# Kernel tuning notes

Measured on AMD Instinct MI355X. Metric: run time of the kernel, lower is better.

The kernel has to match this reference:

```python
import jax, jax.numpy as jnp
import numpy as np

EPS = 1e-3
LOG2PI = float(np.log(2.0 * np.pi))

# dims
B, Z, Y, T, D = 32768, 256, 32, 64, 4  # batch, z_dim, y_dim, n_types, type_dim


def setup_inputs() -> dict:
    key = jax.random.key(0)
    ks = jax.random.split(key, 8)
    z = jax.random.normal(ks[0], (B, Z), dtype=jnp.float32)
    batch_x = jax.random.normal(ks[1], (B, T, D), dtype=jnp.float32)
    miss_list = jax.random.randint(ks[2], (B, T), 0, 2, dtype=jnp.int32)  # 1=observed, 0=missing
    data_mean = jax.random.normal(ks[3], (T, D), dtype=jnp.float32)
    data_var = jax.random.uniform(ks[4], (T, D), dtype=jnp.float32, minval=0.5, maxval=1.5)
    # weights init N(0, 0.005) as in the torch module; biases zero
    Wy = jax.random.normal(ks[5], (T * Y, Z), dtype=jnp.float32) * 0.005
    by = jnp.zeros((T * Y,), dtype=jnp.float32)
    Wm = jax.random.normal(ks[6], (T, D, Y), dtype=jnp.float32) * 0.005
    bm = jnp.zeros((T, D), dtype=jnp.float32)
    Wv = jax.random.normal(ks[7], (T, D, Y), dtype=jnp.float32) * 0.005
    bv = jnp.zeros((T, D), dtype=jnp.float32)
    return {"z": z, "batch_x": batch_x, "miss_list": miss_list,
            "data_mean": data_mean, "data_var": data_var,
            "Wy": Wy, "by": by, "Wm": Wm, "bm": bm, "Wv": Wv, "bv": bv}


def reference(z, batch_x, miss_list, data_mean, data_var, Wy, by, Wm, bm, Wv, bv):
    # y_layer: z -> [B, T*Y], grouped into per-type gamma slices [B, T, Y]
    y = z @ Wy.T + by
    gamma = y.reshape(y.shape[0], T, Y)

    mask = miss_list.astype(gamma.dtype)            # [B, T], 1=observed
    m3 = mask[:, :, None]                           # [B, T, 1]

    # per-type tiny linears (dynamic_partition + Linear + dynamic_stitch).
    # Numerically: same linear on all rows; missing rows are under no_grad,
    # realized here as stop_gradient on the missing partition.
    lin_m = jnp.einsum('bty,tdy->btd', gamma, Wm) + bm   # [B, T, D]
    lin_v = jnp.einsum('bty,tdy->btd', gamma, Wv) + bv
    est_mean = m3 * lin_m + (1.0 - m3) * jax.lax.stop_gradient(lin_m)
    est_var_raw = m3 * lin_v + (1.0 - m3) * jax.lax.stop_gradient(lin_v)

    # loglik_real: softplus variance, denormalize with data mean/var
    dvar = jnp.clip(data_var, EPS)
    est_var = jnp.clip(jax.nn.softplus(est_var_raw), EPS, 1e20)
    mean_x = jnp.sqrt(dvar) * est_mean + data_mean       # [B, T, D]
    var_x = dvar * est_var                               # [B, T, D]

    log_p = -0.5 * jnp.sum((batch_x - mean_x) ** 2 / var_x + jnp.log(var_x) + LOG2PI, axis=-1)  # [B, T]
    log_p_x = log_p * mask
    log_p_x_missing = log_p * (1.0 - mask)
    return (log_p_x, log_p_x_missing, mean_x, var_x)
```

## Files before the change

### kernel.cpp

```cpp
#include <hip/hip_runtime.h>


#define Bsz   32768
#define Tsz   64
#define Dsz   4
#define Ysz   32
#define Zsz   256
#define Nsz   512
#define BTtot (Bsz * Tsz)
#define EPS_  1e-3f
#define LOG2PI_ 1.8378770664093453f

#define BM       32
#define NT       512
#define ASTRIDE  264
#define LSTRIDE  524

typedef __attribute__((ext_vector_type(4))) float  f32x4;
typedef __attribute__((ext_vector_type(8))) short  short8;
typedef __attribute__((ext_vector_type(2))) unsigned int uint2v;

static __device__ __forceinline__ unsigned short f2bf(float f) {
    unsigned int u = __float_as_uint(f);
    return (unsigned short)((u + 0x7fffu + ((u >> 16) & 1u)) >> 16);
}
static __device__ __forceinline__ float bf2f(unsigned short h) {
    return __uint_as_float(((unsigned int)h) << 16);
}
static __device__ __forceinline__ unsigned int cvt_pk_bf16(float a, float b) {
    unsigned int r;
    asm("v_cvt_pk_bf16_f32 %0, %1, %2" : "=v"(r) : "v"(a), "v"(b));
    return r;
}

__global__ __launch_bounds__(256)
void hidec_prep(const float* __restrict__ Wy, const float* __restrict__ by,
                const float* __restrict__ Wm, const float* __restrict__ bm,
                const float* __restrict__ Wv, const float* __restrict__ bv,
                unsigned short* __restrict__ weff, float* __restrict__ beff) {
    __shared__ float Ml[8][Ysz];
    __shared__ float byl[Ysz];
    const int t   = blockIdx.x;
    const int tid = threadIdx.x;
    {
        int j = tid >> 5, y = tid & 31;
        const float* src = (j < 4) ? Wm : Wv;
        Ml[j][y] = src[(t * Dsz + (j & 3)) * Ysz + y];
    }
    if (tid < Ysz) byl[tid] = by[t * Ysz + tid];
    __syncthreads();

    const int k = tid;
    const int kk = k >> 5, q = (k >> 3) & 3, je = k & 7;
    float wy[Ysz];
#pragma unroll
    for (int y = 0; y < Ysz; ++y)
        wy[y] = Wy[(size_t)(t * Ysz + y) * Zsz + k];
#pragma unroll
    for (int j = 0; j < 8; ++j) {
        float acc = 0.f;
#pragma unroll
        for (int y = 0; y < Ysz; ++y) acc = fmaf(Ml[j][y], wy[y], acc);
        int n   = t * 8 + j;
        int tau = n >> 4, c = n & 15;
        weff[((((tau * 8 + kk) * 4 + q) * 16 + c) * 8) + je] = f2bf(acc);
    }
    if (tid < 8) {
        int d = tid & 3;
        float s = ((tid < 4) ? bm : bv)[t * Dsz + d];
        for (int y = 0; y < Ysz; ++y) s = fmaf(byl[y], Ml[tid][y], s);
        beff[t * 8 + tid] = s;
    }
}

__global__ __launch_bounds__(NT, 8)
void hidec_main(const float* __restrict__ z, const float* __restrict__ bx,
                const int* __restrict__ miss, const float* __restrict__ dmean,
                const float* __restrict__ dvarp, const unsigned short* __restrict__ weff,
                const float* __restrict__ beff, float* __restrict__ out) {
    __shared__ unsigned short buf[BM * LSTRIDE];

    const int tid  = threadIdx.x;
    const long row0 = (long)blockIdx.x * BM;

    unsigned short* a_lds = buf;
#pragma unroll
    for (int i = 0; i < 4; ++i) {
        int idx4 = tid + i * NT;
        int r  = idx4 >> 6;
        int c4 = idx4 & 63;
        float4 v = *(const float4*)(z + (row0 + r) * Zsz + c4 * 4);
        uint2v pk;
        pk.x = cvt_pk_bf16(v.x, v.y);
        pk.y = cvt_pk_bf16(v.z, v.w);
        *(uint2v*)&a_lds[r * ASTRIDE + c4 * 4] = pk;
    }
    __syncthreads();

    const int lane = tid & 63;
    const int w    = tid >> 6;
    const int c    = lane & 15;
    const int q    = lane >> 4;

    f32x4 acc[8];
#pragma unroll
    for (int i = 0; i < 8; ++i) acc[i] = (f32x4){0.f, 0.f, 0.f, 0.f};

    const unsigned short* wp = weff + ((size_t)(w * 4) * 8) * 512 + lane * 8;

#pragma unroll
    for (int kk = 0; kk < 8; ++kk) {
        short8 b0 = *(const short8*)(wp + kk * 512 + 0 * 4096);
        short8 b1 = *(const short8*)(wp + kk * 512 + 1 * 4096);
        short8 b2 = *(const short8*)(wp + kk * 512 + 2 * 4096);
        short8 b3 = *(const short8*)(wp + kk * 512 + 3 * 4096);
        short8 a0 = *(const short8*)&a_lds[(0 * 16 + c) * ASTRIDE + kk * 32 + q * 8];
        short8 a1 = *(const short8*)&a_lds[(1 * 16 + c) * ASTRIDE + kk * 32 + q * 8];
        acc[0] = __builtin_amdgcn_mfma_f32_16x16x32_bf16(a0, b0, acc[0], 0, 0, 0);
        acc[1] = __builtin_amdgcn_mfma_f32_16x16x32_bf16(a1, b0, acc[1], 0, 0, 0);
        acc[2] = __builtin_amdgcn_mfma_f32_16x16x32_bf16(a0, b1, acc[2], 0, 0, 0);
        acc[3] = __builtin_amdgcn_mfma_f32_16x16x32_bf16(a1, b1, acc[3], 0, 0, 0);
        acc[4] = __builtin_amdgcn_mfma_f32_16x16x32_bf16(a0, b2, acc[4], 0, 0, 0);
        acc[5] = __builtin_amdgcn_mfma_f32_16x16x32_bf16(a1, b2, acc[5], 0, 0, 0);
        acc[6] = __builtin_amdgcn_mfma_f32_16x16x32_bf16(a0, b3, acc[6], 0, 0, 0);
        acc[7] = __builtin_amdgcn_mfma_f32_16x16x32_bf16(a1, b3, acc[7], 0, 0, 0);
    }
    __syncthreads();

    unsigned short* lin = buf;
    {
        float bb[4];
#pragma unroll
        for (int ti = 0; ti < 4; ++ti) bb[ti] = beff[w * 64 + ti * 16 + c];
#pragma unroll
        for (int h = 0; h < 2; ++h) {
#pragma unroll
            for (int ti = 0; ti < 4; ++ti) {
                int cb = w * 64 + ti * 16 + c;
                const f32x4 a = acc[ti * 2 + h];
                unsigned int p01 = cvt_pk_bf16(a[0] + bb[ti], a[1] + bb[ti]);
                unsigned int p23 = cvt_pk_bf16(a[2] + bb[ti], a[3] + bb[ti]);
                int rbase = h * 16 + q * 4;
                lin[(rbase + 0) * LSTRIDE + cb] = (unsigned short)(p01 & 0xffffu);
                lin[(rbase + 1) * LSTRIDE + cb] = (unsigned short)(p01 >> 16);
                lin[(rbase + 2) * LSTRIDE + cb] = (unsigned short)(p23 & 0xffffu);
                lin[(rbase + 3) * LSTRIDE + cb] = (unsigned short)(p23 >> 16);
            }
        }
    }
    __syncthreads();

    const int t = lane;
    float4 dv4 = *(const float4*)(dvarp + t * 4);
    float4 dm4 = *(const float4*)(dmean + t * 4);
    float dca[4] = {fmaxf(dv4.x, EPS_), fmaxf(dv4.y, EPS_),
                    fmaxf(dv4.z, EPS_), fmaxf(dv4.w, EPS_)};
    float sqa[4] = {sqrtf(dca[0]), sqrtf(dca[1]), sqrtf(dca[2]), sqrtf(dca[3])};
    float dma[4] = {dm4.x, dm4.y, dm4.z, dm4.w};
    float sldv = __logf(dca[0]) + __logf(dca[1]) + __logf(dca[2]) + __logf(dca[3]);

#pragma unroll
    for (int pp = 0; pp < 4; ++pp) {
        int rl  = pp * 8 + w;
        long bt = (row0 + rl) * Tsz + t;

        short8 l8 = *(const short8*)&lin[rl * LSTRIDE + t * 8];
        float lm[4], lv[4];
#pragma unroll
        for (int d = 0; d < 4; ++d) {
            lm[d] = bf2f((unsigned short)l8[d]);
            lv[d] = bf2f((unsigned short)l8[4 + d]);
        }

        float4 x4  = *(const float4*)(bx + bt * 4);
        float mk   = (float)miss[bt];
        float xa[4]  = {x4.x,  x4.y,  x4.z,  x4.w};

        float mean_o[4], var_o[4];
        float s = sldv;
        float evp = 1.f;
#pragma unroll
        for (int d = 0; d < 4; ++d) {
            float mean = fmaf(sqa[d], lm[d], dma[d]);
            float v    = lv[d];
            float sp   = fmaxf(v, 0.f) + __logf(1.f + __expf(-fabsf(v)));
            float ev   = fminf(fmaxf(sp, EPS_), 1e20f);
            float var  = dca[d] * ev;
            float diff = xa[d] - mean;
            s = fmaf(diff * diff, __builtin_amdgcn_rcpf(var), s);
            evp *= ev;
            mean_o[d] = mean;
            var_o[d]  = var;
        }
        s += __logf(evp);
        float logp = -0.5f * (s + 4.f * LOG2PI_);

        float lx = logp * mk;
        out[bt]         = lx;
        out[BTtot + bt] = logp - lx;

        *(float4*)(out + 2L * BTtot + bt * 4) =
            (float4){mean_o[0], mean_o[1], mean_o[2], mean_o[3]};
        *(float4*)(out + 6L * BTtot + bt * 4) =
            (float4){var_o[0], var_o[1], var_o[2], var_o[3]};
    }
}

extern "C" void kernel_launch(void* const* d_in, const int* in_sizes, int n_in,
                              void* d_out, int out_size, void* d_ws, size_t ws_size,
                              hipStream_t stream) {
    const float* z     = (const float*)d_in[0];
    const float* bx    = (const float*)d_in[1];
    const int*   miss  = (const int*)d_in[2];
    const float* dmean = (const float*)d_in[3];
    const float* dvar  = (const float*)d_in[4];
    const float* Wy    = (const float*)d_in[5];
    const float* by    = (const float*)d_in[6];
    const float* Wm    = (const float*)d_in[7];
    const float* bm    = (const float*)d_in[8];
    const float* Wv    = (const float*)d_in[9];
    const float* bv    = (const float*)d_in[10];
    float* out = (float*)d_out;

    unsigned short* weff = (unsigned short*)d_ws;
    float* beff = (float*)((char*)d_ws + (size_t)Nsz * Zsz * 2);

    hidec_prep<<<Tsz, Zsz, 0, stream>>>(Wy, by, Wm, bm, Wv, bv, weff, beff);
    hidec_main<<<Bsz / BM, NT, 0, stream>>>(z, bx, miss, dmean, dvar, weff, beff, out);
}
```

Before: 182.1 us.

## Double-buffer z tiles across two row blocks per workgroup with prefetch

Each workgroup now handles two 32-row tiles. The z loads for the second tile are issued before the first tile's MFMA loop and written to a second LDS buffer afterwards. The epilogue is split into two 16-row halves that reuse the current buffer, and batch_x and miss loads are hoisted ahead of the LDS staging. The aim is to hide global load latency behind compute and to amortise per-block setup (data_var, bias and log terms). In exchange the LDS footprint per block is larger, occupancy drops (launch bounds lowered to 4), there are more barriers, and the grid is half as large.

```diff
diff --git a/kernel.cpp b/kernel.cpp
--- a/kernel.cpp
+++ b/kernel.cpp
@@ -15,6 +15,7 @@
 #define NT       512
 #define ASTRIDE  264
 #define LSTRIDE  524
+#define BUFSZ    8448
 
 typedef __attribute__((ext_vector_type(4))) float  f32x4;
 typedef __attribute__((ext_vector_type(8))) short  short8;
@@ -73,82 +74,20 @@
     }
 }
 
-__global__ __launch_bounds__(NT, 8)
+__global__ __launch_bounds__(NT, 4)
 void hidec_main(const float* __restrict__ z, const float* __restrict__ bx,
                 const int* __restrict__ miss, const float* __restrict__ dmean,
                 const float* __restrict__ dvarp, const unsigned short* __restrict__ weff,
                 const float* __restrict__ beff, float* __restrict__ out) {
-    __shared__ unsigned short buf[BM * LSTRIDE];
+    __shared__ unsigned short buf[2 * BUFSZ];
 
     const int tid  = threadIdx.x;
-    const long row0 = (long)blockIdx.x * BM;
-
-    unsigned short* a_lds = buf;
-#pragma unroll
-    for (int i = 0; i < 4; ++i) {
-        int idx4 = tid + i * NT;
-        int r  = idx4 >> 6;
-        int c4 = idx4 & 63;
-        float4 v = *(const float4*)(z + (row0 + r) * Zsz + c4 * 4);
-        uint2v pk;
-        pk.x = cvt_pk_bf16(v.x, v.y);
-        pk.y = cvt_pk_bf16(v.z, v.w);
-        *(uint2v*)&a_lds[r * ASTRIDE + c4 * 4] = pk;
-    }
-    __syncthreads();
-
     const int lane = tid & 63;
     const int w    = tid >> 6;
     const int c    = lane & 15;
     const int q    = lane >> 4;
-
-    f32x4 acc[8];
-#pragma unroll
-    for (int i = 0; i < 8; ++i) acc[i] = (f32x4){0.f, 0.f, 0.f, 0.f};
-
-    const unsigned short* wp = weff + ((size_t)(w * 4) * 8) * 512 + lane * 8;
-
-#pragma unroll
-    for (int kk = 0; kk < 8; ++kk) {
-        short8 b0 = *(const short8*)(wp + kk * 512 + 0 * 4096);
-        short8 b1 = *(const short8*)(wp + kk * 512 + 1 * 4096);
-        short8 b2 = *(const short8*)(wp + kk * 512 + 2 * 4096);
-        short8 b3 = *(const short8*)(wp + kk * 512 + 3 * 4096);
-        short8 a0 = *(const short8*)&a_lds[(0 * 16 + c) * ASTRIDE + kk * 32 + q * 8];
-        short8 a1 = *(const short8*)&a_lds[(1 * 16 + c) * ASTRIDE + kk * 32 + q * 8];
-        acc[0] = __builtin_amdgcn_mfma_f32_16x16x32_bf16(a0, b0, acc[0], 0, 0, 0);
-        acc[1] = __builtin_amdgcn_mfma_f32_16x16x32_bf16(a1, b0, acc[1], 0, 0, 0);
-        acc[2] = __builtin_amdgcn_mfma_f32_16x16x32_bf16(a0, b1, acc[2], 0, 0, 0);
-        acc[3] = __builtin_amdgcn_mfma_f32_16x16x32_bf16(a1, b1, acc[3], 0, 0, 0);
-        acc[4] = __builtin_amdgcn_mfma_f32_16x16x32_bf16(a0, b2, acc[4], 0, 0, 0);
-        acc[5] = __builtin_amdgcn_mfma_f32_16x16x32_bf16(a1, b2, acc[5], 0, 0, 0);
-        acc[6] = __builtin_amdgcn_mfma_f32_16x16x32_bf16(a0, b3, acc[6], 0, 0, 0);
-        acc[7] = __builtin_amdgcn_mfma_f32_16x16x32_bf16(a1, b3, acc[7], 0, 0, 0);
-    }
-    __syncthreads();
-
-    unsigned short* lin = buf;
-    {
-        float bb[4];
-#pragma unroll
-        for (int ti = 0; ti < 4; ++ti) bb[ti] = beff[w * 64 + ti * 16 + c];
-#pragma unroll
-        for (int h = 0; h < 2; ++h) {
-#pragma unroll
-            for (int ti = 0; ti < 4; ++ti) {
-                int cb = w * 64 + ti * 16 + c;
-                const f32x4 a = acc[ti * 2 + h];
-                unsigned int p01 = cvt_pk_bf16(a[0] + bb[ti], a[1] + bb[ti]);
-                unsigned int p23 = cvt_pk_bf16(a[2] + bb[ti], a[3] + bb[ti]);
-                int rbase = h * 16 + q * 4;
-                lin[(rbase + 0) * LSTRIDE + cb] = (unsigned short)(p01 & 0xffffu);
-                lin[(rbase + 1) * LSTRIDE + cb] = (unsigned short)(p01 >> 16);
-                lin[(rbase + 2) * LSTRIDE + cb] = (unsigned short)(p23 & 0xffffu);
-                lin[(rbase + 3) * LSTRIDE + cb] = (unsigned short)(p23 >> 16);
-            }
-        }
-    }
-    __syncthreads();
+    const long brow0 = (long)blockIdx.x * (2 * BM);
+
 
     const int t = lane;
     float4 dv4 = *(const float4*)(dvarp + t * 4);
@@ -158,51 +97,155 @@
     float sqa[4] = {sqrtf(dca[0]), sqrtf(dca[1]), sqrtf(dca[2]), sqrtf(dca[3])};
     float dma[4] = {dm4.x, dm4.y, dm4.z, dm4.w};
     float sldv = __logf(dca[0]) + __logf(dca[1]) + __logf(dca[2]) + __logf(dca[3]);
-
-#pragma unroll
-    for (int pp = 0; pp < 4; ++pp) {
-        int rl  = pp * 8 + w;
-        long bt = (row0 + rl) * Tsz + t;
-
-        short8 l8 = *(const short8*)&lin[rl * LSTRIDE + t * 8];
-        float lm[4], lv[4];
-#pragma unroll
-        for (int d = 0; d < 4; ++d) {
-            lm[d] = bf2f((unsigned short)l8[d]);
-            lv[d] = bf2f((unsigned short)l8[4 + d]);
-        }
-
-        float4 x4  = *(const float4*)(bx + bt * 4);
-        float mk   = (float)miss[bt];
-        float xa[4]  = {x4.x,  x4.y,  x4.z,  x4.w};
-
-        float mean_o[4], var_o[4];
-        float s = sldv;
-        float evp = 1.f;
-#pragma unroll
-        for (int d = 0; d < 4; ++d) {
-            float mean = fmaf(sqa[d], lm[d], dma[d]);
-            float v    = lv[d];
-            float sp   = fmaxf(v, 0.f) + __logf(1.f + __expf(-fabsf(v)));
-            float ev   = fminf(fmaxf(sp, EPS_), 1e20f);
-            float var  = dca[d] * ev;
-            float diff = xa[d] - mean;
-            s = fmaf(diff * diff, __builtin_amdgcn_rcpf(var), s);
-            evp *= ev;
-            mean_o[d] = mean;
-            var_o[d]  = var;
-        }
-        s += __logf(evp);
-        float logp = -0.5f * (s + 4.f * LOG2PI_);
-
-        float lx = logp * mk;
-        out[bt]         = lx;
-        out[BTtot + bt] = logp - lx;
-
-        *(float4*)(out + 2L * BTtot + bt * 4) =
-            (float4){mean_o[0], mean_o[1], mean_o[2], mean_o[3]};
-        *(float4*)(out + 6L * BTtot + bt * 4) =
-            (float4){var_o[0], var_o[1], var_o[2], var_o[3]};
+    float bb[4];
+#pragma unroll
+    for (int ti = 0; ti < 4; ++ti) bb[ti] = beff[w * 64 + ti * 16 + c];
+
+    float4 zr[4];
+#pragma unroll
+    for (int i = 0; i < 4; ++i) {
+        int idx4 = tid + i * NT;
+        int r = idx4 >> 6, c4 = idx4 & 63;
+        zr[i] = *(const float4*)(z + (brow0 + r) * Zsz + c4 * 4);
+    }
+    {
+        unsigned short* P = buf;
+#pragma unroll
+        for (int i = 0; i < 4; ++i) {
+            int idx4 = tid + i * NT;
+            int r = idx4 >> 6, c4 = idx4 & 63;
+            uint2v pk;
+            pk.x = cvt_pk_bf16(zr[i].x, zr[i].y);
+            pk.y = cvt_pk_bf16(zr[i].z, zr[i].w);
+            *(uint2v*)&P[r * ASTRIDE + c4 * 4] = pk;
+        }
+    }
+    __syncthreads();
+
+    const unsigned short* wp = weff + ((size_t)(w * 4) * 8) * 512 + lane * 8;
+
+#pragma unroll 1
+    for (int it = 0; it < 2; ++it) {
+        unsigned short* cur = buf + (it ? BUFSZ : 0);
+        unsigned short* nxt = buf + (it ? 0 : BUFSZ);
+        const long row0 = brow0 + it * BM;
+
+        if (it == 0) {
+#pragma unroll
+            for (int i = 0; i < 4; ++i) {
+                int idx4 = tid + i * NT;
+                int r = idx4 >> 6, c4 = idx4 & 63;
+                zr[i] = *(const float4*)(z + (brow0 + BM + r) * Zsz + c4 * 4);
+            }
+            __builtin_amdgcn_sched_barrier(0);
+        }
+
+        f32x4 acc[8];
+#pragma unroll
+        for (int i = 0; i < 8; ++i) acc[i] = (f32x4){0.f, 0.f, 0.f, 0.f};
+
+#pragma unroll
+        for (int kk = 0; kk < 8; ++kk) {
+            short8 b0 = *(const short8*)(wp + kk * 512 + 0 * 4096);
+            short8 b1 = *(const short8*)(wp + kk * 512 + 1 * 4096);
+            short8 b2 = *(const short8*)(wp + kk * 512 + 2 * 4096);
+            short8 b3 = *(const short8*)(wp + kk * 512 + 3 * 4096);
+            short8 a0 = *(const short8*)&cur[(0 * 16 + c) * ASTRIDE + kk * 32 + q * 8];
+            short8 a1 = *(const short8*)&cur[(1 * 16 + c) * ASTRIDE + kk * 32 + q * 8];
+            acc[0] = __builtin_amdgcn_mfma_f32_16x16x32_bf16(a0, b0, acc[0], 0, 0, 0);
+            acc[1] = __builtin_amdgcn_mfma_f32_16x16x32_bf16(a1, b0, acc[1], 0, 0, 0);
+            acc[2] = __builtin_amdgcn_mfma_f32_16x16x32_bf16(a0, b1, acc[2], 0, 0, 0);
+            acc[3] = __builtin_amdgcn_mfma_f32_16x16x32_bf16(a1, b1, acc[3], 0, 0, 0);
+            acc[4] = __builtin_amdgcn_mfma_f32_16x16x32_bf16(a0, b2, acc[4], 0, 0, 0);
+            acc[5] = __builtin_amdgcn_mfma_f32_16x16x32_bf16(a1, b2, acc[5], 0, 0, 0);
+            acc[6] = __builtin_amdgcn_mfma_f32_16x16x32_bf16(a0, b3, acc[6], 0, 0, 0);
+            acc[7] = __builtin_amdgcn_mfma_f32_16x16x32_bf16(a1, b3, acc[7], 0, 0, 0);
+        }
+
+        if (it == 0) {
+#pragma unroll
+            for (int i = 0; i < 4; ++i) {
+                int idx4 = tid + i * NT;
+                int r = idx4 >> 6, c4 = idx4 & 63;
+                uint2v pk;
+                pk.x = cvt_pk_bf16(zr[i].x, zr[i].y);
+                pk.y = cvt_pk_bf16(zr[i].z, zr[i].w);
+                *(uint2v*)&nxt[r * ASTRIDE + c4 * 4] = pk;
+            }
+        }
+        __syncthreads();
+
+#pragma unroll
+        for (int h = 0; h < 2; ++h) {
+            float4 xp[2];
+            int    mp[2];
+#pragma unroll
+            for (int pp = 0; pp < 2; ++pp) {
+                long bt = (row0 + h * 16 + pp * 8 + w) * Tsz + t;
+                xp[pp] = *(const float4*)(bx + bt * 4);
+                mp[pp] = miss[bt];
+            }
+
+#pragma unroll
+            for (int ti = 0; ti < 4; ++ti) {
+                int cb = w * 64 + ti * 16 + c;
+                const f32x4 a = acc[ti * 2 + h];
+                unsigned int p01 = cvt_pk_bf16(a[0] + bb[ti], a[1] + bb[ti]);
+                unsigned int p23 = cvt_pk_bf16(a[2] + bb[ti], a[3] + bb[ti]);
+                int rbase = q * 4;
+                cur[(rbase + 0) * LSTRIDE + cb] = (unsigned short)(p01 & 0xffffu);
+                cur[(rbase + 1) * LSTRIDE + cb] = (unsigned short)(p01 >> 16);
+                cur[(rbase + 2) * LSTRIDE + cb] = (unsigned short)(p23 & 0xffffu);
+                cur[(rbase + 3) * LSTRIDE + cb] = (unsigned short)(p23 >> 16);
+            }
+            __syncthreads();
+
+#pragma unroll
+            for (int pp = 0; pp < 2; ++pp) {
+                int rl  = pp * 8 + w;
+                long bt = (row0 + h * 16 + rl) * Tsz + t;
+
+                short8 l8 = *(const short8*)&cur[rl * LSTRIDE + t * 8];
+                float lm[4], lv[4];
+#pragma unroll
+                for (int d = 0; d < 4; ++d) {
+                    lm[d] = bf2f((unsigned short)l8[d]);
+                    lv[d] = bf2f((unsigned short)l8[4 + d]);
+                }
+
+                float mk = (float)mp[pp];
+                float xa[4] = {xp[pp].x, xp[pp].y, xp[pp].z, xp[pp].w};
+
+                float mean_o[4], var_o[4];
+                float s = sldv;
+                float evp = 1.f;
+#pragma unroll
+                for (int d = 0; d < 4; ++d) {
+                    float mean = fmaf(sqa[d], lm[d], dma[d]);
+                    float v    = lv[d];
+                    float sp   = fmaxf(v, 0.f) + __logf(1.f + __expf(-fabsf(v)));
+                    float ev   = fminf(fmaxf(sp, EPS_), 1e20f);
+                    float var  = dca[d] * ev;
+                    float diff = xa[d] - mean;
+                    s = fmaf(diff * diff, __builtin_amdgcn_rcpf(var), s);
+                    evp *= ev;
+                    mean_o[d] = mean;
+                    var_o[d]  = var;
+                }
+                s += __logf(evp);
+                float logp = -0.5f * (s + 4.f * LOG2PI_);
+
+                float lx = logp * mk;
+                out[bt]         = lx;
+                out[BTtot + bt] = logp - lx;
+
+                *(float4*)(out + 2L * BTtot + bt * 4) =
+                    (float4){mean_o[0], mean_o[1], mean_o[2], mean_o[3]};
+                *(float4*)(out + 6L * BTtot + bt * 4) =
+                    (float4){var_o[0], var_o[1], var_o[2], var_o[3]};
+            }
+            __syncthreads();
+        }
     }
 }
 
@@ -226,5 +269,5 @@
     float* beff = (float*)((char*)d_ws + (size_t)Nsz * Zsz * 2);
 
     hidec_prep<<<Tsz, Zsz, 0, stream>>>(Wy, by, Wm, bm, Wv, bv, weff, beff);
-    hidec_main<<<Bsz / BM, NT, 0, stream>>>(z, bx, miss, dmean, dvar, weff, beff, out);
-}
+    hidec_main<<<Bsz / (2 * BM), NT, 0, stream>>>(z, bx, miss, dmean, dvar, weff, beff, out);
+}
```

Result: slower. 230.0 us (+26.3%).
